# Performance work log

Measured on AMD Instinct MI355X. Metric: run time of the kernel, lower is better.

## Reference

```python
import jax, jax.numpy as jnp
import numpy as np

N = 100000       # nodes
E = 1_600_000    # edges (before self-loops)
NFEAT = 128
NHID = 32
HEADS = 4
HID = NHID * HEADS   # 128
NCLASS = 40
EPS = 1e-5
NEG = 0.2            # leaky_relu negative slope (GATConv default)


def setup_inputs() -> dict:
    key = jax.random.key(0)
    ks = jax.random.split(key, 32)
    s = 0.1
    d = {}
    d["x"] = jax.random.normal(ks[0], (N, NFEAT), jnp.float32)
    d["edge_index"] = jax.random.randint(ks[1], (2, E), 0, N, jnp.int32)
    # conv0: nfeat -> nhid, heads=4, concat
    d["W0"] = jax.random.normal(ks[2], (HID, NFEAT), jnp.float32) * s
    d["as0"] = jax.random.normal(ks[3], (HEADS, NHID), jnp.float32) * s
    d["ad0"] = jax.random.normal(ks[4], (HEADS, NHID), jnp.float32) * s
    d["b0"] = jnp.zeros((HID,), jnp.float32)
    d["g0"] = jnp.ones((HID,), jnp.float32)
    d["be0"] = jnp.zeros((HID,), jnp.float32)
    d["m0"] = jax.random.normal(ks[5], (HID,), jnp.float32) * 0.01
    d["v0"] = jax.random.uniform(ks[6], (HID,), jnp.float32, 0.5, 1.5)
    # conv1: hid -> nhid, heads=4, concat
    d["W1"] = jax.random.normal(ks[7], (HID, HID), jnp.float32) * s
    d["as1"] = jax.random.normal(ks[8], (HEADS, NHID), jnp.float32) * s
    d["ad1"] = jax.random.normal(ks[9], (HEADS, NHID), jnp.float32) * s
    d["b1"] = jnp.zeros((HID,), jnp.float32)
    d["g1"] = jnp.ones((HID,), jnp.float32)
    d["be1"] = jnp.zeros((HID,), jnp.float32)
    d["m1"] = jax.random.normal(ks[10], (HID,), jnp.float32) * 0.01
    d["v1"] = jax.random.uniform(ks[11], (HID,), jnp.float32, 0.5, 1.5)
    # conv_out: hid -> nclass, heads=1, concat=False
    d["W2"] = jax.random.normal(ks[12], (NCLASS, HID), jnp.float32) * s
    d["as2"] = jax.random.normal(ks[13], (1, NCLASS), jnp.float32) * s
    d["ad2"] = jax.random.normal(ks[14], (1, NCLASS), jnp.float32) * s
    d["b2"] = jnp.zeros((NCLASS,), jnp.float32)
    return d


def _gat(x, W, a_s, a_d, bias, src, dst, n, concat):
    # PyG GATConv: project, per-head attention logits, segment softmax over dst, scatter-sum
    H, C = a_s.shape
    h = (x @ W.T).reshape(n, H, C)                      # [N,H,C]
    al_s = jnp.einsum('nhc,hc->nh', h, a_s)             # [N,H]
    al_d = jnp.einsum('nhc,hc->nh', h, a_d)
    e = al_s[src] + al_d[dst]                           # [E,H]
    e = jnp.where(e > 0, e, NEG * e)                    # leaky_relu
    m = jax.ops.segment_max(e, dst, num_segments=n)     # self-loops guarantee nonempty segments
    ex = jnp.exp(e - m[dst])
    ssum = jax.ops.segment_sum(ex, dst, num_segments=n)
    alpha = ex / ssum[dst]                              # [E,H]
    out = jax.ops.segment_sum(alpha[:, :, None] * h[src], dst, num_segments=n)  # [N,H,C]
    out = out.reshape(n, H * C) if concat else out.mean(axis=1)
    return out + bias


def _bn_eval(x, g, b, m, v):
    return (x - m) * jax.lax.rsqrt(v + EPS) * g + b


def reference(x, edge_index, W0, as0, ad0, b0, g0, be0, m0, v0,
              W1, as1, ad1, b1, g1, be1, m1, v1, W2, as2, ad2, b2):
    n = x.shape[0]
    loop = jnp.arange(n, dtype=edge_index.dtype)
    src = jnp.concatenate([edge_index[0], loop])        # add_self_loops=True (PyG default)
    dst = jnp.concatenate([edge_index[1], loop])
    h = _gat(x, W0, as0, ad0, b0, src, dst, n, True)
    h = jax.nn.relu(_bn_eval(h, g0, be0, m0, v0))       # dropout is identity in eval
    h = _gat(h, W1, as1, ad1, b1, src, dst, n, True)
    h = jax.nn.relu(_bn_eval(h, g1, be1, m1, v1))
    h = _gat(h, W2, as2, ad2, b2, src, dst, n, False)
    return jax.nn.log_softmax(h, axis=1)
```

## Files before the change

### kernel.cpp

```cpp
#include <hip/hip_runtime.h>
#include <math.h>

#define NEGS 0.2f
#define EPSBN 1e-5f
#define NBIN_MAX 256
#define SBITS 9
#define SNODES 512
#define GLH 256

typedef __attribute__((ext_vector_type(8))) short short8v;
typedef __attribute__((ext_vector_type(4))) float f32x4;

static __device__ __forceinline__ float lrelu(float x){ return x > 0.f ? x : NEGS*x; }
static __device__ __forceinline__ float bf_lo(unsigned u){ return __uint_as_float(u << 16); }
static __device__ __forceinline__ float bf_hi(unsigned u){ return __uint_as_float(u & 0xffff0000u); }
static __device__ __forceinline__ float bf1(unsigned short v){ return __uint_as_float(((unsigned)v) << 16); }
static __device__ __forceinline__ unsigned short f2bf(float f){
  unsigned u = __float_as_uint(f);
  unsigned r = (u + 0x7fff + ((u >> 16) & 1)) >> 16;
  return (unsigned short)r;
}

__global__ void k_prep(const float* __restrict__ W0, const float* __restrict__ W1,
                       const float* __restrict__ W2, unsigned short* __restrict__ Wb0,
                       unsigned short* __restrict__ Wb1, float* __restrict__ Wt2p){
  int i = blockIdx.x*256 + threadIdx.x;
  if (i < 16384){ Wb0[i] = f2bf(W0[i]); return; }
  if (i < 32768){ Wb1[i-16384] = f2bf(W1[i-16384]); return; }
  if (i < 40960){
    int j = i - 32768;
    int k = j >> 6, c = j & 63;
    Wt2p[j] = (c < 40) ? W2[c*128 + k] : 0.f;
  }
}

__global__ void k_scan1(const int* __restrict__ in, int* __restrict__ incl,
                        int* __restrict__ partials, int n){
  __shared__ int sd[256];
  int tid = threadIdx.x;
  int base = blockIdx.x*1024 + tid*4;
  int v[4]; int s = 0;
  #pragma unroll
  for (int j=0;j<4;++j){ int idx = base+j; v[j] = (idx<n)? in[idx] : 0; s += v[j]; }
  sd[tid] = s; __syncthreads();
  for (int off=1; off<256; off<<=1){
    int t = (tid>=off)? sd[tid-off] : 0;
    __syncthreads();
    sd[tid] += t;
    __syncthreads();
  }
  int run = sd[tid] - s;
  #pragma unroll
  for (int j=0;j<4;++j){ int idx = base+j; run += v[j]; if (idx<n) incl[idx] = run; }
  if (tid==255) partials[blockIdx.x] = sd[255];
}

__global__ void k_scan2(int* partials, int nb){
  __shared__ int sd[256];
  int tid = threadIdx.x;
  sd[tid] = (tid<nb)? partials[tid] : 0;
  __syncthreads();
  for (int off=1; off<256; off<<=1){
    int t = (tid>=off)? sd[tid-off] : 0;
    __syncthreads();
    sd[tid] += t;
    __syncthreads();
  }
  if (tid<nb) partials[tid] = sd[tid];
}

__global__ void k_scan3(int* __restrict__ offs, const int* __restrict__ partials, int n){
  int i = blockIdx.x*256 + threadIdx.x;
  if (i == 0) offs[0] = 0;
  if (i >= n) return;
  int b = i >> 10;
  if (b > 0) offs[i+1] += partials[b-1];
}

__global__ __launch_bounds__(256) void k_lhist(const int* __restrict__ ei, int E, int N,
                                               int* __restrict__ Hmat, int nbin){
  __shared__ int lh[NBIN_MAX];
  int tid = threadIdx.x;
  lh[tid] = 0;
  __syncthreads();
  int ET = E + N;
  int c0 = (int)(((long long)ET * blockIdx.x) / GLH);
  int c1 = (int)(((long long)ET * (blockIdx.x+1)) / GLH);
  for (int i = c0 + tid; i < c1; i += 256){
    int d = (i < E) ? ei[E + i] : (i - E);
    atomicAdd(&lh[d >> SBITS], 1);
  }
  __syncthreads();
  for (int b = tid; b < nbin; b += 256)
    Hmat[b*GLH + blockIdx.x] = lh[b];
}

__global__ __launch_bounds__(256) void k_write(const int* __restrict__ ei, int E, int N,
                        const int* __restrict__ Bmat, unsigned* __restrict__ staged, int nbin){
  __shared__ int cur[NBIN_MAX];
  int tid = threadIdx.x;
  for (int b = tid; b < nbin; b += 256)
    cur[b] = Bmat[b*GLH + blockIdx.x];
  __syncthreads();
  int ET = E + N;
  int c0 = (int)(((long long)ET * blockIdx.x) / GLH);
  int c1 = (int)(((long long)ET * (blockIdx.x+1)) / GLH);
  for (int i = c0 + tid; i < c1; i += 256){
    int s, d;
    if (i < E){ s = ei[i]; d = ei[E+i]; } else { s = i-E; d = i-E; }
    int pos = atomicAdd(&cur[d >> SBITS], 1);
    staged[pos] = (unsigned)s | ((unsigned)(d & (SNODES-1)) << 23);
  }
}

__global__ __launch_bounds__(256) void k_bucket3(const unsigned* __restrict__ staged,
                         const int* __restrict__ Bmat,
                         int* __restrict__ offs, int* __restrict__ csr, int N, int ET){
  __shared__ int sdeg[SNODES];
  __shared__ int sexc[SNODES];
  int b = blockIdx.x, tid = threadIdx.x;
  int node0 = b << SBITS;
  int nn = min(SNODES, N - node0);
  int base = Bmat[b*GLH];
  int cntb = Bmat[(b+1)*GLH] - base;
  sdeg[2*tid] = 0; sdeg[2*tid+1] = 0;
  __syncthreads();
  for (int e = tid; e < cntb; e += 256){
    unsigned p = staged[base + e];
    atomicAdd(&sdeg[p >> 23], 1);
  }
  __syncthreads();
  int v0 = sdeg[2*tid], v1 = sdeg[2*tid+1];
  int ps = v0 + v1;
  sexc[tid] = ps; __syncthreads();
  for (int off=1; off<256; off<<=1){
    int t = (tid>=off)? sexc[tid-off] : 0;
    __syncthreads();
    sexc[tid] += t;
    __syncthreads();
  }
  int excl_pair = sexc[tid] - ps;
  __syncthreads();
  sexc[2*tid]   = excl_pair;
  sexc[2*tid+1] = excl_pair + v0;
  if (2*tid   < nn) offs[node0 + 2*tid]   = base + excl_pair;
  if (2*tid+1 < nn) offs[node0 + 2*tid+1] = base + excl_pair + v0;
  sdeg[2*tid] = 0; sdeg[2*tid+1] = 0;
  __syncthreads();
  for (int e = tid; e < cntb; e += 256){
    unsigned p = staged[base + e];
    int ln = p >> 23;
    int pos = base + sexc[ln] + atomicAdd(&sdeg[ln], 1);
    csr[pos] = (int)(p & 0x7FFFFFu);
  }
  if (b == gridDim.x - 1 && tid == 0) offs[N] = ET;
}

template<bool BF16IN>
__global__ __launch_bounds__(256) void k_gemm128m(const void* __restrict__ Xin,
                          const unsigned short* __restrict__ Wb,
                          const float* __restrict__ as_, const float* __restrict__ ad_,
                          unsigned short* __restrict__ Yb,
                          float* __restrict__ ALs, float* __restrict__ ALd, int n){
  __shared__ short lds[24576];
  unsigned* ldsW = (unsigned*)lds;
  unsigned* ldsX = (unsigned*)(lds + 16384);
  int tid = threadIdx.x;
  int r0 = blockIdx.x*64;
  #pragma unroll
  for (int j=0;j<8;++j){
    int dw4 = 1024*j + tid*4;
    int row = dw4 >> 6;
    uint4 v = *(const uint4*)(Wb + (size_t)dw4*2);
    int lo = dw4 & 63, base = dw4 & ~63;
    *(uint4*)(&ldsW[base | (lo ^ ((row&7)<<2))]) = v;
  }
  if (!BF16IN){
    const float* X = (const float*)Xin;
    #pragma unroll
    for (int j=0;j<8;++j){
      int i = (256*j + tid)*4;
      int row = i >> 7;
      int grow = r0 + row;
      float4 v = (grow < n) ? *(const float4*)(X + (size_t)grow*128 + (i&127))
                            : make_float4(0.f,0.f,0.f,0.f);
      int dw = i >> 1, lo = dw & 63, base = dw & ~63;
      int sw = base | (lo ^ ((row&7)<<2));
      uint2 p;
      p.x = (unsigned)f2bf(v.x) | ((unsigned)f2bf(v.y)<<16);
      p.y = (unsigned)f2bf(v.z) | ((unsigned)f2bf(v.w)<<16);
      *(uint2*)(&ldsX[sw]) = p;
    }
  } else {
    const unsigned short* Xb = (const unsigned short*)Xin;
    #pragma unroll
    for (int j=0;j<4;++j){
      int dw4 = 1024*j + tid*4;
      int row = dw4 >> 6;
      int grow = r0 + row;
      uint4 v = (grow < n) ? *(const uint4*)(Xb + (size_t)grow*128 + (dw4&63)*2)
                           : make_uint4(0,0,0,0);
      int lo = dw4 & 63, base = dw4 & ~63;
      int sw = base | (lo ^ ((row&7)<<2));
      *(uint4*)(&ldsX[sw]) = v;
    }
  }
  __syncthreads();
  int l = tid & 63, w = tid >> 6;
  int lrow = l & 15, lk = l >> 4;
  int arow = w*16 + lrow;
  int abase = arow*64, ax = (arow&7)<<2;
  short8v a[4];
  #pragma unroll
  for (int ks=0;ks<4;++ks){
    int lo = ks*16 + lk*4;
    a[ks] = *(const short8v*)&ldsX[abase + (lo ^ ax)];
  }
  f32x4 acc[8];
  #pragma unroll
  for (int c=0;c<8;++c) acc[c] = (f32x4){0.f,0.f,0.f,0.f};
  #pragma unroll
  for (int c=0;c<8;++c){
    int brow = c*16 + lrow;
    int bbase2 = brow*64, bx = (brow&7)<<2;
    #pragma unroll
    for (int ks=0;ks<4;++ks){
      int lo = ks*16 + lk*4;
      short8v bfr = *(const short8v*)&ldsW[bbase2 + (lo ^ bx)];
      acc[c] = __builtin_amdgcn_mfma_f32_16x16x32_bf16(a[ks], bfr, acc[c], 0, 0, 0);
    }
  }
  __syncthreads();
  unsigned short* Ys = (unsigned short*)ldsX;
  #pragma unroll
  for (int c=0;c<8;++c){
    #pragma unroll
    for (int r=0;r<4;++r){
      int row = w*16 + lk*4 + r;
      Ys[row*128 + c*16 + lrow] = f2bf(acc[c][r]);
    }
  }
  __syncthreads();
  #pragma unroll
  for (int j=0;j<4;++j){
    int dw4 = 1024*j + tid*4;
    int row = dw4 >> 6;
    int grow = r0 + row;
    if (grow < n)
      *(uint4*)(Yb + (size_t)grow*128 + (dw4&63)*2) = *(const uint4*)&((unsigned*)ldsX)[dw4];
  }
  {
    int row = tid >> 2, h = tid & 3;
    int grow = r0 + row;
    if (grow < n){
      const unsigned short* yr = Ys + row*128 + h*32;
      float ps = 0.f, pd = 0.f;
      #pragma unroll
      for (int j=0;j<32;++j){
        float y = bf1(yr[j]);
        ps = fmaf(y, as_[h*32+j], ps);
        pd = fmaf(y, ad_[h*32+j], pd);
      }
      ALs[grow*4+h] = ps; ALd[grow*4+h] = pd;
    }
  }
}

__global__ __launch_bounds__(256) void k_agg128b(const unsigned short* __restrict__ Pb,
                         const float* __restrict__ ALs, const float* __restrict__ ALd,
                         const int* __restrict__ offs, const int* __restrict__ csr,
                         const float* __restrict__ bias, const float* __restrict__ gam,
                         const float* __restrict__ bet, const float* __restrict__ mean,
                         const float* __restrict__ var, unsigned short* __restrict__ outb, int n){
  int node = blockIdx.x*4 + (threadIdx.x >> 6);
  int lane = threadIdx.x & 63;
  if (node >= n) return;
  int el = lane >> 4, fl = lane & 15, hd = fl >> 2;
  int beg = offs[node], end = offs[node+1];
  int deg = end - beg;
  float aldw = ALd[node*4 + (lane & 3)];
  int c = (lane < deg) ? csr[beg + lane] : 0;
  float w0, w1, w2, w3;
  {
    int e0 = lane >> 2, h0 = lane & 3;
    int s0 = __shfl(c, e0), s1 = __shfl(c, 16+e0);
    int s2 = __shfl(c, 32+e0), s3 = __shfl(c, 48+e0);
    float al0 = ALs[s0*4+h0], al1 = ALs[s1*4+h0];
    float al2 = ALs[s2*4+h0], al3 = ALs[s3*4+h0];
    w0 = (e0      < deg) ? __expf(lrelu(al0 + aldw)) : 0.f;
    w1 = (16 + e0 < deg) ? __expf(lrelu(al1 + aldw)) : 0.f;
    w2 = (32 + e0 < deg) ? __expf(lrelu(al2 + aldw)) : 0.f;
    w3 = (48 + e0 < deg) ? __expf(lrelu(al3 + aldw)) : 0.f;
  }
  float a0=0.f,a1=0.f,a2=0.f,a3=0.f,a4=0.f,a5=0.f,a6=0.f,a7=0.f;
  float wsum = 0.f;
  int nsteps = (deg + 3) >> 2;
  int ns64 = min(nsteps, 16);
  uint4 hv;
  {
    int si = __shfl(c, el);
    hv = *(const uint4*)(Pb + (size_t)si*128 + fl*8);
  }
  for (int st = 0; st < ns64; ++st){
    int q = st >> 2, r = st & 3;
    float wc = (q==0) ? w0 : (q==1) ? w1 : (q==2) ? w2 : w3;
    float w = __shfl(wc, (r*4 + el)*4 + hd);
    uint4 hvN = make_uint4(0,0,0,0);
    if (st + 1 < ns64){
      int siN = __shfl(c, (st+1)*4 + el);
      hvN = *(const uint4*)(Pb + (size_t)siN*128 + fl*8);
    }
    wsum += w;
    a0 = fmaf(w, bf_lo(hv.x), a0);  a1 = fmaf(w, bf_hi(hv.x), a1);
    a2 = fmaf(w, bf_lo(hv.y), a2);  a3 = fmaf(w, bf_hi(hv.y), a3);
    a4 = fmaf(w, bf_lo(hv.z), a4);  a5 = fmaf(w, bf_hi(hv.z), a5);
    a6 = fmaf(w, bf_lo(hv.w), a6);  a7 = fmaf(w, bf_hi(hv.w), a7);
    hv = hvN;
  }
  if (deg > 64){
    float aldh = __shfl(aldw, hd);
    for (int idx = 64 + el; idx < deg; idx += 4){
      int si = csr[beg + idx];
      float w = __expf(lrelu(ALs[si*4 + hd] + aldh));
      uint4 h4 = *(const uint4*)(Pb + (size_t)si*128 + fl*8);
      wsum += w;
      a0 = fmaf(w, bf_lo(h4.x), a0);  a1 = fmaf(w, bf_hi(h4.x), a1);
      a2 = fmaf(w, bf_lo(h4.y), a2);  a3 = fmaf(w, bf_hi(h4.y), a3);
      a4 = fmaf(w, bf_lo(h4.z), a4);  a5 = fmaf(w, bf_hi(h4.z), a5);
      a6 = fmaf(w, bf_lo(h4.w), a6);  a7 = fmaf(w, bf_hi(h4.w), a7);
    }
  }
  #pragma unroll
  for (int off=16; off<64; off<<=1){
    a0 += __shfl_xor(a0, off); a1 += __shfl_xor(a1, off);
    a2 += __shfl_xor(a2, off); a3 += __shfl_xor(a3, off);
    a4 += __shfl_xor(a4, off); a5 += __shfl_xor(a5, off);
    a6 += __shfl_xor(a6, off); a7 += __shfl_xor(a7, off);
    wsum += __shfl_xor(wsum, off);
  }
  if (el == 0){
    float inv = 1.f / wsum;
    int cc = fl*8;
    float4 bA = *(const float4*)(bias+cc), bB = *(const float4*)(bias+cc+4);
    float4 gA = *(const float4*)(gam+cc),  gB = *(const float4*)(gam+cc+4);
    float4 eA = *(const float4*)(bet+cc),  eB = *(const float4*)(bet+cc+4);
    float4 uA = *(const float4*)(mean+cc), uB = *(const float4*)(mean+cc+4);
    float4 vA = *(const float4*)(var+cc),  vB = *(const float4*)(var+cc+4);
    float o0 = (a0*inv + bA.x - uA.x) * rsqrtf(vA.x + EPSBN) * gA.x + eA.x;
    float o1 = (a1*inv + bA.y - uA.y) * rsqrtf(vA.y + EPSBN) * gA.y + eA.y;
    float o2 = (a2*inv + bA.z - uA.z) * rsqrtf(vA.z + EPSBN) * gA.z + eA.z;
    float o3 = (a3*inv + bA.w - uA.w) * rsqrtf(vA.w + EPSBN) * gA.w + eA.w;
    float o4 = (a4*inv + bB.x - uB.x) * rsqrtf(vB.x + EPSBN) * gB.x + eB.x;
    float o5 = (a5*inv + bB.y - uB.y) * rsqrtf(vB.y + EPSBN) * gB.y + eB.y;
    float o6 = (a6*inv + bB.z - uB.z) * rsqrtf(vB.z + EPSBN) * gB.z + eB.z;
    float o7 = (a7*inv + bB.w - uB.w) * rsqrtf(vB.w + EPSBN) * gB.w + eB.w;
    uint4 q;
    q.x = (unsigned)f2bf(fmaxf(o0,0.f)) | ((unsigned)f2bf(fmaxf(o1,0.f))<<16);
    q.y = (unsigned)f2bf(fmaxf(o2,0.f)) | ((unsigned)f2bf(fmaxf(o3,0.f))<<16);
    q.z = (unsigned)f2bf(fmaxf(o4,0.f)) | ((unsigned)f2bf(fmaxf(o5,0.f))<<16);
    q.w = (unsigned)f2bf(fmaxf(o6,0.f)) | ((unsigned)f2bf(fmaxf(o7,0.f))<<16);
    *(uint4*)(outb + (size_t)node*128 + cc) = q;
  }
}

__global__ __launch_bounds__(256) void k_gemm40n(const unsigned short* __restrict__ Gb,
                                                 const float* __restrict__ Wt2p,
                                                 const float* __restrict__ as2,
                                                 const float* __restrict__ ad2,
                                                 unsigned short* __restrict__ H2b,
                                                 float* __restrict__ al2s,
                                                 float* __restrict__ al2d, int n){
  __shared__ float xt[128*68];
  int tid = threadIdx.x;
  int r0 = blockIdx.x * 64;
  {
    int r  = tid & 63;
    int c0 = (tid >> 6) * 32;
    int row = r0 + r;
    #pragma unroll
    for (int j=0;j<4;++j){
      uint4 v = (row < n) ? *(const uint4*)(Gb + (size_t)row*128 + c0 + j*8)
                          : make_uint4(0,0,0,0);
      int k = c0 + j*8;
      xt[(k+0)*68 + r] = bf_lo(v.x);  xt[(k+1)*68 + r] = bf_hi(v.x);
      xt[(k+2)*68 + r] = bf_lo(v.y);  xt[(k+3)*68 + r] = bf_hi(v.y);
      xt[(k+4)*68 + r] = bf_lo(v.z);  xt[(k+5)*68 + r] = bf_hi(v.z);
      xt[(k+6)*68 + r] = bf_lo(v.w);  xt[(k+7)*68 + r] = bf_hi(v.w);
    }
  }
  __syncthreads();
  int tc = tid & 15, tr = tid >> 4;
  float acc[4][4] = {};
  #pragma unroll 4
  for (int k=0;k<128;++k){
    float4 wv = *(const float4*)(Wt2p + k*64 + tc*4);
    float4 xv = *(const float4*)(&xt[k*68 + tr*4]);
    float xv4[4] = {xv.x, xv.y, xv.z, xv.w};
    float wv4[4] = {wv.x, wv.y, wv.z, wv.w};
    #pragma unroll
    for (int u=0;u<4;++u)
      #pragma unroll
      for (int v=0;v<4;++v)
        acc[u][v] = fmaf(xv4[u], wv4[v], acc[u][v]);
  }
  float4 a4 = make_float4(0.f,0.f,0.f,0.f), d4 = a4;
  if (tc < 10){
    a4 = *(const float4*)(as2 + tc*4);
    d4 = *(const float4*)(ad2 + tc*4);
  }
  #pragma unroll
  for (int u=0;u<4;++u){
    int row = r0 + tr*4 + u;
    float ps = acc[u][0]*a4.x + acc[u][1]*a4.y + acc[u][2]*a4.z + acc[u][3]*a4.w;
    float pd = acc[u][0]*d4.x + acc[u][1]*d4.y + acc[u][2]*d4.z + acc[u][3]*d4.w;
    #pragma unroll
    for (int m=1; m<16; m<<=1){ ps += __shfl_xor(ps,m); pd += __shfl_xor(pd,m); }
    if (row < n){
      if (tc < 10){
        ushort4 o;
        o.x = f2bf(acc[u][0]); o.y = f2bf(acc[u][1]);
        o.z = f2bf(acc[u][2]); o.w = f2bf(acc[u][3]);
        *(ushort4*)(H2b + (size_t)row*40 + tc*4) = o;
      }
      if (tc == 0){ al2s[row] = ps; al2d[row] = pd; }
    }
  }
}

__global__ __launch_bounds__(256) void k_agg40b(const unsigned short* __restrict__ H2b,
                        const float* __restrict__ ALs, const float* __restrict__ ALd,
                        const int* __restrict__ offs, const int* __restrict__ csr,
                        const float* __restrict__ b2, float* __restrict__ out, int n){
  int node = blockIdx.x*4 + (threadIdx.x >> 6);
  int lane = threadIdx.x & 63;
  if (node >= n) return;
  int el = lane >> 3, fl = lane & 7;
  bool act = fl < 5;
  int beg = offs[node], end = offs[node+1];
  int deg = end - beg;
  float ald = ALd[node];
  int c = (lane < deg) ? csr[beg + lane] : 0;
  float wch = (lane < deg) ? __expf(lrelu(ALs[c] + ald)) : 0.f;
  float a0=0.f,a1=0.f,a2=0.f,a3=0.f,a4=0.f,a5=0.f,a6=0.f,a7=0.f;
  float wsum = 0.f;
  int nsteps = (deg + 7) >> 3;
  int ns64 = min(nsteps, 8);
  uint4 hv = make_uint4(0,0,0,0);
  {
    int si = __shfl(c, el);
    if (act) hv = *(const uint4*)(H2b + (size_t)si*40 + fl*8);
  }
  for (int st = 0; st < ns64; ++st){
    float w = __shfl(wch, st*8 + el);
    uint4 hvN = make_uint4(0,0,0,0);
    if (st + 1 < ns64){
      int siN = __shfl(c, (st+1)*8 + el);
      if (act) hvN = *(const uint4*)(H2b + (size_t)siN*40 + fl*8);
    }
    wsum += w;
    a0 = fmaf(w, bf_lo(hv.x), a0);  a1 = fmaf(w, bf_hi(hv.x), a1);
    a2 = fmaf(w, bf_lo(hv.y), a2);  a3 = fmaf(w, bf_hi(hv.y), a3);
    a4 = fmaf(w, bf_lo(hv.z), a4);  a5 = fmaf(w, bf_hi(hv.z), a5);
    a6 = fmaf(w, bf_lo(hv.w), a6);  a7 = fmaf(w, bf_hi(hv.w), a7);
    hv = hvN;
  }
  if (deg > 64){
    for (int idx = 64 + el; idx < deg; idx += 8){
      int si = csr[beg + idx];
      float w = __expf(lrelu(ALs[si] + ald));
      wsum += w;
      if (act){
        uint4 h4 = *(const uint4*)(H2b + (size_t)si*40 + fl*8);
        a0 = fmaf(w, bf_lo(h4.x), a0);  a1 = fmaf(w, bf_hi(h4.x), a1);
        a2 = fmaf(w, bf_lo(h4.y), a2);  a3 = fmaf(w, bf_hi(h4.y), a3);
        a4 = fmaf(w, bf_lo(h4.z), a4);  a5 = fmaf(w, bf_hi(h4.z), a5);
        a6 = fmaf(w, bf_lo(h4.w), a6);  a7 = fmaf(w, bf_hi(h4.w), a7);
      }
    }
  }
  #pragma unroll
  for (int off=8; off<64; off<<=1){
    a0 += __shfl_xor(a0, off); a1 += __shfl_xor(a1, off);
    a2 += __shfl_xor(a2, off); a3 += __shfl_xor(a3, off);
    a4 += __shfl_xor(a4, off); a5 += __shfl_xor(a5, off);
    a6 += __shfl_xor(a6, off); a7 += __shfl_xor(a7, off);
    wsum += __shfl_xor(wsum, off);
  }
  if (el == 0){
    float inv = 1.f / wsum;
    float y0=0.f,y1=0.f,y2=0.f,y3=0.f,y4=0.f,y5=0.f,y6=0.f,y7=0.f;
    if (act){
      int cc = fl*8;
      float4 bA = *(const float4*)(b2 + cc), bB = *(const float4*)(b2 + cc + 4);
      y0 = a0*inv + bA.x; y1 = a1*inv + bA.y; y2 = a2*inv + bA.z; y3 = a3*inv + bA.w;
      y4 = a4*inv + bB.x; y5 = a5*inv + bB.y; y6 = a6*inv + bB.z; y7 = a7*inv + bB.w;
    }
    float lm = act ? fmaxf(fmaxf(fmaxf(y0,y1),fmaxf(y2,y3)),
                           fmaxf(fmaxf(y4,y5),fmaxf(y6,y7))) : -1e30f;
    lm = fmaxf(lm, __shfl_xor(lm,1));
    lm = fmaxf(lm, __shfl_xor(lm,2));
    lm = fmaxf(lm, __shfl_xor(lm,4));
    float ls = act ? (__expf(y0-lm)+__expf(y1-lm)+__expf(y2-lm)+__expf(y3-lm)
                     +__expf(y4-lm)+__expf(y5-lm)+__expf(y6-lm)+__expf(y7-lm)) : 0.f;
    ls += __shfl_xor(ls,1);
    ls += __shfl_xor(ls,2);
    ls += __shfl_xor(ls,4);
    float lg = lm + __logf(ls);
    if (act){
      float4* dst = (float4*)(out + (size_t)node*40 + fl*8);
      dst[0] = make_float4(y0-lg, y1-lg, y2-lg, y3-lg);
      dst[1] = make_float4(y4-lg, y5-lg, y6-lg, y7-lg);
    }
  }
}

extern "C" void kernel_launch(void* const* d_in, const int* in_sizes, int n_in,
                              void* d_out, int out_size, void* d_ws, size_t ws_size,
                              hipStream_t stream) {
  const float* x   = (const float*)d_in[0];
  const int*   ei  = (const int*)d_in[1];
  const float* W0  = (const float*)d_in[2];
  const float* as0 = (const float*)d_in[3];
  const float* ad0 = (const float*)d_in[4];
  const float* b0  = (const float*)d_in[5];
  const float* g0  = (const float*)d_in[6];
  const float* be0 = (const float*)d_in[7];
  const float* m0  = (const float*)d_in[8];
  const float* v0  = (const float*)d_in[9];
  const float* W1  = (const float*)d_in[10];
  const float* as1 = (const float*)d_in[11];
  const float* ad1 = (const float*)d_in[12];
  const float* b1  = (const float*)d_in[13];
  const float* g1  = (const float*)d_in[14];
  const float* be1 = (const float*)d_in[15];
  const float* m1  = (const float*)d_in[16];
  const float* v1  = (const float*)d_in[17];
  const float* W2  = (const float*)d_in[18];
  const float* as2 = (const float*)d_in[19];
  const float* ad2 = (const float*)d_in[20];
  const float* b2  = (const float*)d_in[21];
  float* out = (float*)d_out;

  int N = in_sizes[0] / 128;
  int E = in_sizes[1] / 2;
  int ET = E + N;
  int NBIN = (N + SNODES - 1) >> SBITS;
  int M = NBIN * GLH;

  char* p = (char*)d_ws;
  auto alloc = [&](size_t bytes)->void* {
    void* r = (void*)p;
    p += (bytes + 255) & ~size_t(255);
    return r;
  };
  unsigned short* Wb0 = (unsigned short*)alloc((size_t)128*128*2);
  unsigned short* Wb1 = (unsigned short*)alloc((size_t)128*128*2);
  float* Wt2p  = (float*)alloc((size_t)128*64*4);
  int* offs    = (int*)alloc((size_t)(N+1)*4);
  int* partials= (int*)alloc(1024*4);
  int* Hmat    = (int*)alloc((size_t)NBIN_MAX*GLH*4);
  int* Bmat    = (int*)alloc((size_t)(NBIN_MAX*GLH+1)*4);
  int* csr     = (int*)alloc((size_t)ET*4);
  unsigned* staged = (unsigned*)alloc((size_t)ET*4);
  unsigned short* Pb = (unsigned short*)alloc((size_t)N*128*2);
  unsigned short* Gb = (unsigned short*)alloc((size_t)N*128*2);
  float* ALs = (float*)alloc((size_t)N*4*4);
  float* ALd = (float*)alloc((size_t)N*4*4);
  unsigned short* H2b = Pb;
  float* al2s = ALs;
  float* al2d = ALd;
  if ((size_t)(p - (char*)d_ws) > ws_size) return;

  k_prep<<<(40960+255)/256, 256, 0, stream>>>(W0, W1, W2, Wb0, Wb1, Wt2p);

  k_lhist<<<GLH, 256, 0, stream>>>(ei, E, N, Hmat, NBIN);
  int nb2 = (M + 1023) / 1024;
  k_scan1<<<nb2, 256, 0, stream>>>(Hmat, Bmat+1, partials, M);
  k_scan2<<<1, 256, 0, stream>>>(partials, nb2);
  k_scan3<<<(M+255)/256, 256, 0, stream>>>(Bmat, partials, M);
  k_write<<<GLH, 256, 0, stream>>>(ei, E, N, Bmat, staged, NBIN);
  k_bucket3<<<NBIN, 256, 0, stream>>>(staged, Bmat, offs, csr, N, ET);

  int gb = (N + 63) / 64;
  k_gemm128m<false><<<gb, 256, 0, stream>>>(x, Wb0, as0, ad0, Pb, ALs, ALd, N);
  k_agg128b<<<(N+3)/4, 256, 0, stream>>>(Pb, ALs, ALd, offs, csr, b0, g0, be0, m0, v0, Gb, N);

  k_gemm128m<true><<<gb, 256, 0, stream>>>(Gb, Wb1, as1, ad1, Pb, ALs, ALd, N);
  k_agg128b<<<(N+3)/4, 256, 0, stream>>>(Pb, ALs, ALd, offs, csr, b1, g1, be1, m1, v1, Gb, N);

  k_gemm40n<<<gb, 256, 0, stream>>>(Gb, Wt2p, as2, ad2, H2b, al2s, al2d, N);
  k_agg40b<<<(N+3)/4, 256, 0, stream>>>(H2b, al2s, al2d, offs, csr, b2, out, N);
}
```

Baseline: 481.6 us.

## Merge weight prep into histogram kernel and deepen gather prefetch in aggregators

Folds the weight conversion kernel into the edge histogram kernel as extra blocks, which removes one launch. The 128-wide and 40-wide aggregation loops now prefetch two neighbor rows ahead instead of one, and the loops are fully unrolled with a double buffer. Accumulation uses 2-wide float vectors so the compiler can emit packed FMA. The deeper prefetch raises register pressure and could reduce occupancy.

```diff
diff --git a/kernel.cpp b/kernel.cpp
--- a/kernel.cpp
+++ b/kernel.cpp
@@ -10,6 +10,7 @@
 
 typedef __attribute__((ext_vector_type(8))) short short8v;
 typedef __attribute__((ext_vector_type(4))) float f32x4;
+typedef __attribute__((ext_vector_type(2))) float f32x2;
 
 static __device__ __forceinline__ float lrelu(float x){ return x > 0.f ? x : NEGS*x; }
 static __device__ __forceinline__ float bf_lo(unsigned u){ return __uint_as_float(u << 16); }
@@ -21,17 +22,36 @@
   return (unsigned short)r;
 }
 
-__global__ void k_prep(const float* __restrict__ W0, const float* __restrict__ W1,
+__global__ __launch_bounds__(256) void k_lhist_prep(const int* __restrict__ ei, int E, int N,
+                       int* __restrict__ Hmat, int nbin,
+                       const float* __restrict__ W0, const float* __restrict__ W1,
                        const float* __restrict__ W2, unsigned short* __restrict__ Wb0,
                        unsigned short* __restrict__ Wb1, float* __restrict__ Wt2p){
-  int i = blockIdx.x*256 + threadIdx.x;
-  if (i < 16384){ Wb0[i] = f2bf(W0[i]); return; }
-  if (i < 32768){ Wb1[i-16384] = f2bf(W1[i-16384]); return; }
-  if (i < 40960){
-    int j = i - 32768;
-    int k = j >> 6, c = j & 63;
-    Wt2p[j] = (c < 40) ? W2[c*128 + k] : 0.f;
-  }
+  if (blockIdx.x >= GLH){
+    int i = (blockIdx.x - GLH)*256 + threadIdx.x;
+    if (i < 16384){ Wb0[i] = f2bf(W0[i]); return; }
+    if (i < 32768){ Wb1[i-16384] = f2bf(W1[i-16384]); return; }
+    if (i < 40960){
+      int j = i - 32768;
+      int k = j >> 6, c = j & 63;
+      Wt2p[j] = (c < 40) ? W2[c*128 + k] : 0.f;
+    }
+    return;
+  }
+  __shared__ int lh[NBIN_MAX];
+  int tid = threadIdx.x;
+  lh[tid] = 0;
+  __syncthreads();
+  int ET = E + N;
+  int c0 = (int)(((long long)ET * blockIdx.x) / GLH);
+  int c1 = (int)(((long long)ET * (blockIdx.x+1)) / GLH);
+  for (int i = c0 + tid; i < c1; i += 256){
+    int d = (i < E) ? ei[E + i] : (i - E);
+    atomicAdd(&lh[d >> SBITS], 1);
+  }
+  __syncthreads();
+  for (int b = tid; b < nbin; b += 256)
+    Hmat[b*GLH + blockIdx.x] = lh[b];
 }
 
 __global__ void k_scan1(const int* __restrict__ in, int* __restrict__ incl,
@@ -75,24 +95,6 @@
   if (i >= n) return;
   int b = i >> 10;
   if (b > 0) offs[i+1] += partials[b-1];
-}
-
-__global__ __launch_bounds__(256) void k_lhist(const int* __restrict__ ei, int E, int N,
-                                               int* __restrict__ Hmat, int nbin){
-  __shared__ int lh[NBIN_MAX];
-  int tid = threadIdx.x;
-  lh[tid] = 0;
-  __syncthreads();
-  int ET = E + N;
-  int c0 = (int)(((long long)ET * blockIdx.x) / GLH);
-  int c1 = (int)(((long long)ET * (blockIdx.x+1)) / GLH);
-  for (int i = c0 + tid; i < c1; i += 256){
-    int d = (i < E) ? ei[E + i] : (i - E);
-    atomicAdd(&lh[d >> SBITS], 1);
-  }
-  __syncthreads();
-  for (int b = tid; b < nbin; b += 256)
-    Hmat[b*GLH + blockIdx.x] = lh[b];
 }
 
 __global__ __launch_bounds__(256) void k_write(const int* __restrict__ ei, int E, int N,
@@ -292,31 +294,39 @@
     w2 = (32 + e0 < deg) ? __expf(lrelu(al2 + aldw)) : 0.f;
     w3 = (48 + e0 < deg) ? __expf(lrelu(al3 + aldw)) : 0.f;
   }
-  float a0=0.f,a1=0.f,a2=0.f,a3=0.f,a4=0.f,a5=0.f,a6=0.f,a7=0.f;
+  f32x2 A0 = (f32x2){0.f,0.f}, A1 = A0, A2 = A0, A3 = A0;
   float wsum = 0.f;
   int nsteps = (deg + 3) >> 2;
   int ns64 = min(nsteps, 16);
-  uint4 hv;
+  uint4 p0, p1;
   {
-    int si = __shfl(c, el);
-    hv = *(const uint4*)(Pb + (size_t)si*128 + fl*8);
-  }
-  for (int st = 0; st < ns64; ++st){
-    int q = st >> 2, r = st & 3;
-    float wc = (q==0) ? w0 : (q==1) ? w1 : (q==2) ? w2 : w3;
-    float w = __shfl(wc, (r*4 + el)*4 + hd);
-    uint4 hvN = make_uint4(0,0,0,0);
-    if (st + 1 < ns64){
-      int siN = __shfl(c, (st+1)*4 + el);
-      hvN = *(const uint4*)(Pb + (size_t)siN*128 + fl*8);
+    int s0i = __shfl(c, el);
+    p0 = *(const uint4*)(Pb + (size_t)s0i*128 + fl*8);
+  }
+  if (ns64 > 1){
+    int s1i = __shfl(c, 4 + el);
+    p1 = *(const uint4*)(Pb + (size_t)s1i*128 + fl*8);
+  } else p1 = make_uint4(0,0,0,0);
+  #pragma unroll
+  for (int st = 0; st < 16; ++st){
+    if (st >= ns64) break;
+    uint4 cur = (st & 1) ? p1 : p0;
+    float wc = (st>>2)==0 ? w0 : (st>>2)==1 ? w1 : (st>>2)==2 ? w2 : w3;
+    float w = __shfl(wc, ((st&3)*4 + el)*4 + hd);
+    uint4 nxt = make_uint4(0,0,0,0);
+    if (st + 2 < ns64){
+      int sN = __shfl(c, (st+2)*4 + el);
+      nxt = *(const uint4*)(Pb + (size_t)sN*128 + fl*8);
     }
     wsum += w;
-    a0 = fmaf(w, bf_lo(hv.x), a0);  a1 = fmaf(w, bf_hi(hv.x), a1);
-    a2 = fmaf(w, bf_lo(hv.y), a2);  a3 = fmaf(w, bf_hi(hv.y), a3);
-    a4 = fmaf(w, bf_lo(hv.z), a4);  a5 = fmaf(w, bf_hi(hv.z), a5);
-    a6 = fmaf(w, bf_lo(hv.w), a6);  a7 = fmaf(w, bf_hi(hv.w), a7);
-    hv = hvN;
-  }
+    f32x2 wv = (f32x2){w, w};
+    A0 += (f32x2){bf_lo(cur.x), bf_hi(cur.x)} * wv;
+    A1 += (f32x2){bf_lo(cur.y), bf_hi(cur.y)} * wv;
+    A2 += (f32x2){bf_lo(cur.z), bf_hi(cur.z)} * wv;
+    A3 += (f32x2){bf_lo(cur.w), bf_hi(cur.w)} * wv;
+    if (st & 1) p1 = nxt; else p0 = nxt;
+  }
+  float a0=A0.x, a1=A0.y, a2=A1.x, a3=A1.y, a4=A2.x, a5=A2.y, a6=A3.x, a7=A3.y;
   if (deg > 64){
     float aldh = __shfl(aldw, hd);
     for (int idx = 64 + el; idx < deg; idx += 4){
@@ -441,29 +451,38 @@
   float ald = ALd[node];
   int c = (lane < deg) ? csr[beg + lane] : 0;
   float wch = (lane < deg) ? __expf(lrelu(ALs[c] + ald)) : 0.f;
-  float a0=0.f,a1=0.f,a2=0.f,a3=0.f,a4=0.f,a5=0.f,a6=0.f,a7=0.f;
+  f32x2 A0 = (f32x2){0.f,0.f}, A1 = A0, A2 = A0, A3 = A0;
   float wsum = 0.f;
   int nsteps = (deg + 7) >> 3;
   int ns64 = min(nsteps, 8);
-  uint4 hv = make_uint4(0,0,0,0);
+  uint4 p0 = make_uint4(0,0,0,0), p1 = p0;
   {
     int si = __shfl(c, el);
-    if (act) hv = *(const uint4*)(H2b + (size_t)si*40 + fl*8);
-  }
-  for (int st = 0; st < ns64; ++st){
+    if (act) p0 = *(const uint4*)(H2b + (size_t)si*40 + fl*8);
+  }
+  if (ns64 > 1){
+    int si = __shfl(c, 8 + el);
+    if (act) p1 = *(const uint4*)(H2b + (size_t)si*40 + fl*8);
+  }
+  #pragma unroll
+  for (int st = 0; st < 8; ++st){
+    if (st >= ns64) break;
+    uint4 cur = (st & 1) ? p1 : p0;
     float w = __shfl(wch, st*8 + el);
-    uint4 hvN = make_uint4(0,0,0,0);
-    if (st + 1 < ns64){
-      int siN = __shfl(c, (st+1)*8 + el);
-      if (act) hvN = *(const uint4*)(H2b + (size_t)siN*40 + fl*8);
+    uint4 nxt = make_uint4(0,0,0,0);
+    if (st + 2 < ns64){
+      int sN = __shfl(c, (st+2)*8 + el);
+      if (act) nxt = *(const uint4*)(H2b + (size_t)sN*40 + fl*8);
     }
     wsum += w;
-    a0 = fmaf(w, bf_lo(hv.x), a0);  a1 = fmaf(w, bf_hi(hv.x), a1);
-    a2 = fmaf(w, bf_lo(hv.y), a2);  a3 = fmaf(w, bf_hi(hv.y), a3);
-    a4 = fmaf(w, bf_lo(hv.z), a4);  a5 = fmaf(w, bf_hi(hv.z), a5);
-    a6 = fmaf(w, bf_lo(hv.w), a6);  a7 = fmaf(w, bf_hi(hv.w), a7);
-    hv = hvN;
-  }
+    f32x2 wv = (f32x2){w, w};
+    A0 += (f32x2){bf_lo(cur.x), bf_hi(cur.x)} * wv;
+    A1 += (f32x2){bf_lo(cur.y), bf_hi(cur.y)} * wv;
+    A2 += (f32x2){bf_lo(cur.z), bf_hi(cur.z)} * wv;
+    A3 += (f32x2){bf_lo(cur.w), bf_hi(cur.w)} * wv;
+    if (st & 1) p1 = nxt; else p0 = nxt;
+  }
+  float a0=A0.x, a1=A0.y, a2=A1.x, a3=A1.y, a4=A2.x, a5=A2.y, a6=A3.x, a7=A3.y;
   if (deg > 64){
     for (int idx = 64 + el; idx < deg; idx += 8){
       int si = csr[beg + idx];
@@ -571,9 +590,7 @@
   float* al2d = ALd;
   if ((size_t)(p - (char*)d_ws) > ws_size) return;
 
-  k_prep<<<(40960+255)/256, 256, 0, stream>>>(W0, W1, W2, Wb0, Wb1, Wt2p);
-
-  k_lhist<<<GLH, 256, 0, stream>>>(ei, E, N, Hmat, NBIN);
+  k_lhist_prep<<<GLH + 160, 256, 0, stream>>>(ei, E, N, Hmat, NBIN, W0, W1, W2, Wb0, Wb1, Wt2p);
   int nb2 = (M + 1023) / 1024;
   k_scan1<<<nb2, 256, 0, stream>>>(Hmat, Bmat+1, partials, M);
   k_scan2<<<1, 256, 0, stream>>>(partials, nb2);
```

Measured after the change: 475.4 us. About the same (-1.3%).
